# Optimization experiments

Measured on AMD Instinct MI355X. Metric: run time of the kernel, lower is better.

## Reference

```python
import jax, jax.numpy as jnp
import numpy as np
from functools import partial

B, T_OUT, T_IN, L, D_IN, D_ATT = 8, 256, 512, 128, 128, 128


def setup_inputs() -> dict:
    key = jax.random.key(0)
    ks = jax.random.split(key, 8)
    s = 0.05  # small init scale for numerical stability
    return {
        "inputs": jax.random.normal(ks[0], (B, T_OUT, D_IN), jnp.float32),
        "attended_inputs": jax.random.normal(ks[1], (B, T_IN, D_ATT), jnp.float32),
        "lstm_kernel": jax.random.normal(ks[2], (D_IN, 4 * L), jnp.float32) * s,
        "lstm_rec_kernel": jax.random.normal(ks[3], (L, 4 * L), jnp.float32) * s,
        "lstm_bias": jnp.zeros((4 * L,), jnp.float32),
        "W1": jax.random.normal(ks[4], (D_ATT, L), jnp.float32) * s,
        "b1": jnp.zeros((L,), jnp.float32),
        "W2": jax.random.normal(ks[5], (L, L), jnp.float32) * s,
        "b2": jnp.zeros((L,), jnp.float32),
        "W3": jax.random.normal(ks[6], (L, 1), jnp.float32) * s,
        "b3": jnp.zeros((1,), jnp.float32),
    }


def _lstm(x, Wk, Wr, b):
    # x: (B, T, D_in). Keras gate order: i, f, c(g), o. Zero initial state.
    Bq = x.shape[0]
    h0 = jnp.zeros((Bq, L), x.dtype)
    c0 = jnp.zeros((Bq, L), x.dtype)
    xz = jnp.einsum('btd,dk->btk', x, Wk) + b  # precompute input projection

    def step(carry, zt):
        h, c = carry
        z = zt + h @ Wr
        i, f, g, o = jnp.split(z, 4, axis=-1)
        c_new = jax.nn.sigmoid(f) * c + jax.nn.sigmoid(i) * jnp.tanh(g)
        h_new = jax.nn.sigmoid(o) * jnp.tanh(c_new)
        return (h_new, c_new), h_new

    (h_T, c_T), hs = jax.lax.scan(step, (h0, c0), jnp.swapaxes(xz, 0, 1))
    return jnp.swapaxes(hs, 0, 1), h_T, c_T  # (B, T, L), (B, L), (B, L)


def reference(inputs, attended_inputs, lstm_kernel, lstm_rec_kernel, lstm_bias,
              W1, b1, W2, b2, W3, b3):
    # setup_attended: keys = dense1(attended_inputs)
    keys = attended_inputs @ W1 + b1  # (B, T_in, L)
    x, h, c = _lstm(inputs, lstm_kernel, lstm_rec_kernel, lstm_bias)  # (B, T_out, L)
    q = x @ W2 + b2  # (B, T_out, L)
    # Bahdanau additive score: tanh(keys[:,None] + q[:,:,None]) . W3 -> (B, T_out, T_in)
    t = jnp.tanh(keys[:, None, :, :] + q[:, :, None, :])  # (B, T_out, T_in, L)
    scores = jnp.einsum('bqkl,l->bqk', t, W3[:, 0]) + b3[0]
    attn = jax.nn.softmax(scores, axis=-1)
    weighted = jnp.einsum('bqk,bkd->bqd', attn, attended_inputs)  # (B, T_out, D_att)
    out = jnp.concatenate([x, weighted], axis=2)  # (B, T_out, L + D_att)
    return out, h, c
```

## Files before the change

### kernel.cpp

```cpp
#include <hip/hip_runtime.h>
#include <hip/hip_bf16.h>

#define XF_OFF   0
#define PROG_OFF 524288
#define XZ_OFF   1048576
#define KEYS_OFF 2097152
#define OUT_H    524288
#define OUT_C    525312

#define LDS_BARRIER() __asm__ __volatile__("s_waitcnt lgkmcnt(0)\n\ts_barrier" ::: "memory")

#if __has_builtin(__builtin_amdgcn_exp2f)
#define EXP2F __builtin_amdgcn_exp2f
#else
#define EXP2F exp2f
#endif

typedef _Float16 f16x8 __attribute__((ext_vector_type(8)));
typedef float fx4 __attribute__((ext_vector_type(4)));

__device__ __forceinline__ float fast_rcp(float x) { return __builtin_amdgcn_rcpf(x); }
__device__ __forceinline__ float fast_sig(float v) { return fast_rcp(1.f + __expf(-v)); }
__device__ __forceinline__ float fast_tanh(float v) { return 2.f * fast_rcp(1.f + __expf(-2.f * v)) - 1.f; }

#define CSCALE (-2.8853900817779268f)

__global__ __launch_bounds__(256)
void prologue_k(const float* __restrict__ inp, const float* __restrict__ Wk,
                const float* __restrict__ bias, const float* __restrict__ att,
                const float* __restrict__ W1, const float* __restrict__ b1,
                float* __restrict__ ws) {
  __shared__ float ar[8][128];
  __shared__ float ar2[16][128];
  const int tid = threadIdx.x;

  if (blockIdx.x < 256) {
    _Float16* xz16 = (_Float16*)(ws + XZ_OFF);
    const int row0 = blockIdx.x * 8;
    for (int i = tid; i < 8 * 128; i += 256) ar[i >> 7][i & 127] = inp[row0 * 128 + i];
    __syncthreads();
    float acc[8][2];
    const float bb0 = bias[tid], bb1 = bias[tid + 256];
#pragma unroll
    for (int r = 0; r < 8; ++r) { acc[r][0] = bb0; acc[r][1] = bb1; }
    for (int d = 0; d < 128; d += 4) {
      float w0a = Wk[(d + 0) * 512 + tid], w0b = Wk[(d + 0) * 512 + tid + 256];
      float w1a = Wk[(d + 1) * 512 + tid], w1b = Wk[(d + 1) * 512 + tid + 256];
      float w2a = Wk[(d + 2) * 512 + tid], w2b = Wk[(d + 2) * 512 + tid + 256];
      float w3a = Wk[(d + 3) * 512 + tid], w3b = Wk[(d + 3) * 512 + tid + 256];
#pragma unroll
      for (int r = 0; r < 8; ++r) {
        float4 a4 = *(const float4*)&ar[r][d];
        acc[r][0] += a4.x * w0a + a4.y * w1a + a4.z * w2a + a4.w * w3a;
        acc[r][1] += a4.x * w0b + a4.y * w1b + a4.z * w2b + a4.w * w3b;
      }
    }
    const int u = tid & 127, g0 = tid >> 7;
#pragma unroll
    for (int r = 0; r < 8; ++r) {
      const int row = row0 + r, b = row >> 8, t = row & 255;
      const int base = ((t * 8 + b) * 128 + u) * 4;
      xz16[base + g0]     = (_Float16)acc[r][0];
      xz16[base + g0 + 2] = (_Float16)acc[r][1];
    }
    return;
  }

  if (blockIdx.x == 256 && tid < 2) ((int*)(ws + PROG_OFF))[tid] = 0;
  const int kb = blockIdx.x - 256;
  const int row0 = kb * 16;
  const int bq = row0 >> 9, k0 = row0 & 511;
  for (int i = tid; i < 16 * 128; i += 256) ar2[i >> 7][i & 127] = att[row0 * 128 + i];
  __syncthreads();
  const int l = tid & 127, r0 = tid >> 7;
  float acc[8];
  const float bl = b1[l];
#pragma unroll
  for (int i = 0; i < 8; ++i) acc[i] = bl;
  for (int d = 0; d < 128; d += 4) {
    float w0 = W1[(d + 0) * 128 + l], w1 = W1[(d + 1) * 128 + l];
    float w2 = W1[(d + 2) * 128 + l], w3 = W1[(d + 3) * 128 + l];
#pragma unroll
    for (int i = 0; i < 8; ++i) {
      float4 a4 = *(const float4*)&ar2[r0 * 8 + i][d];
      acc[i] += a4.x * w0 + a4.y * w1 + a4.z * w2 + a4.w * w3;
    }
  }
  float* kT = ws + KEYS_OFF + (bq * 128 + l) * 512 + k0 + r0 * 8;
  float4 lo = {acc[0], acc[1], acc[2], acc[3]};
  float4 hi = {acc[4], acc[5], acc[6], acc[7]};
  *(float4*)kT = lo;
  *(float4*)(kT + 4) = hi;
}

struct ScanS { _Float16 hb[2][576]; };
struct AttnS {
  float xr[4][128];
  float qp[4][128];
  float sc[4][512];
  float kc[8][516];
  float w3s[128];
};

__global__ __launch_bounds__(512)
void fused_scan_attn(const float* __restrict__ Wrf, const float* __restrict__ att,
                     const float* __restrict__ W2c, const float* __restrict__ b2c,
                     const float* __restrict__ W3c, const float* __restrict__ b3c,
                     float* __restrict__ ws, float* __restrict__ out) {
  __shared__ __align__(16) char smem[29312];
  const int tid = threadIdx.x;
  int* prog = (int*)(ws + PROG_OFF);
  float* xf = ws + XF_OFF;

  if (blockIdx.x == 256 || blockIdx.x == 257) return;

  if (blockIdx.x >= 2) {
    AttnS* A = (AttnS*)smem;
    const int wkr = (blockIdx.x < 256) ? (int)blockIdx.x - 2 : (int)blockIdx.x - 4;
    int cA = wkr, cB = 511 - wkr;
    if ((cA & 63) > (cB & 63)) { int tmp = cA; cA = cB; cB = tmp; }
    if (tid < 128) A->w3s[tid] = 2.f * W3c[tid];
    float sw3 = 0.f;
    for (int ll = 0; ll < 128; ll += 4) {
      float4 w4 = *(const float4*)&W3c[ll];
      sw3 += w4.x + w4.y + w4.z + w4.w;
    }
    const int l = tid & 127, r0 = tid >> 7;
    for (int ci = 0; ci < 2; ++ci) {
      const int c = ci ? cB : cA;
      const int b = c >> 6, q0 = (c & 63) * 4;
      if (tid == 0) {
        while (__hip_atomic_load(&prog[b >> 2], __ATOMIC_RELAXED, __HIP_MEMORY_SCOPE_AGENT) < q0 + 4)
          __builtin_amdgcn_s_sleep(16);
      }
      __syncthreads();
      const int row = b * 256 + q0 + r0;
      const float xv = __hip_atomic_load(&xf[row * 128 + l], __ATOMIC_RELAXED, __HIP_MEMORY_SCOPE_AGENT);
      A->xr[r0][l] = xv;
      out[row * 256 + l] = xv;
      __syncthreads();
      float qa = b2c[l];
      for (int d = 0; d < 128; d += 4) {
        float4 x4 = *(const float4*)&A->xr[r0][d];
        qa += x4.x * W2c[(d + 0) * 128 + l] + x4.y * W2c[(d + 1) * 128 + l]
            + x4.z * W2c[(d + 2) * 128 + l] + x4.w * W2c[(d + 3) * 128 + l];
      }
      A->qp[r0][l] = CSCALE * qa;
      const float base = b3c[0] - sw3;
      float acc0 = base, acc1 = base, acc2 = base, acc3 = base;
      const float* keysT = ws + KEYS_OFF + b * (128 * 512);
      for (int cc = 0; cc < 128; cc += 8) {
        __syncthreads();
        for (int i = tid; i < 8 * 512; i += 512)
          A->kc[i >> 9][i & 511] = CSCALE * keysT[(cc + (i >> 9)) * 512 + (i & 511)];
        __syncthreads();
        for (int lp = 0; lp < 8; ++lp) {
          const float qv = A->qp[r0][cc + lp];
          const float wv = A->w3s[cc + lp];
          acc0 += fast_rcp(1.f + EXP2F(A->kc[lp][l]       + qv)) * wv;
          acc1 += fast_rcp(1.f + EXP2F(A->kc[lp][l + 128] + qv)) * wv;
          acc2 += fast_rcp(1.f + EXP2F(A->kc[lp][l + 256] + qv)) * wv;
          acc3 += fast_rcp(1.f + EXP2F(A->kc[lp][l + 384] + qv)) * wv;
        }
      }
      A->sc[r0][l]       = acc0;
      A->sc[r0][l + 128] = acc1;
      A->sc[r0][l + 256] = acc2;
      A->sc[r0][l + 384] = acc3;
      __syncthreads();
      {
        const int wave = tid >> 6, lane = tid & 63;
        if (wave < 4) {
          float v[8];
#pragma unroll
          for (int i = 0; i < 8; ++i) v[i] = A->sc[wave][lane + i * 64];
          float m = v[0];
#pragma unroll
          for (int i = 1; i < 8; ++i) m = fmaxf(m, v[i]);
#pragma unroll
          for (int off = 32; off > 0; off >>= 1) m = fmaxf(m, __shfl_xor(m, off));
          float e[8], s = 0.f;
#pragma unroll
          for (int i = 0; i < 8; ++i) { e[i] = __expf(v[i] - m); s += e[i]; }
#pragma unroll
          for (int off = 32; off > 0; off >>= 1) s += __shfl_xor(s, off);
          const float inv = fast_rcp(s);
#pragma unroll
          for (int i = 0; i < 8; ++i) A->sc[wave][lane + i * 64] = e[i] * inv;
        }
      }
      __syncthreads();
      const float* attb = att + b * (512 * 128);
      float wa = 0.f;
      for (int k = 0; k < 512; k += 4) {
        float4 p4 = *(const float4*)&A->sc[r0][k];
        wa += p4.x * attb[(k + 0) * 128 + l] + p4.y * attb[(k + 1) * 128 + l]
            + p4.z * attb[(k + 2) * 128 + l] + p4.w * attb[(k + 3) * 128 + l];
      }
      out[row * 256 + 128 + l] = wa;
    }
    return;
  }

  __builtin_amdgcn_s_setprio(1);
  ScanS* S = (ScanS*)smem;
  const _Float16* xz16 = (const _Float16*)(ws + XZ_OFF);
  const int b_base = blockIdx.x * 4;
  const int w = tid >> 6, lane = tid & 63;
  const int q = lane >> 4, p = lane & 15;
  const int b = p & 3, isel = p >> 2;
  const int u = 16 * w + 4 * isel + q;
  const int bg = b_base + b;

  f16x8 afr[4][4];
#pragma unroll
  for (int i = 0; i < 4; ++i) {
    const int col = (p & 3) * 128 + 16 * w + 4 * i + (p >> 2);
#pragma unroll
    for (int kt = 0; kt < 4; ++kt)
#pragma unroll
      for (int j = 0; j < 8; ++j)
        afr[i][kt][j] = (_Float16)Wrf[(kt * 32 + q * 8 + j) * 512 + col];
  }
  {
    _Float16* hp = &S->hb[0][0];
    for (int i = tid; i < 2 * 576; i += 512) hp[i] = (_Float16)0.f;
  }
  const fx4 zeroC = {0.f, 0.f, 0.f, 0.f};
  float cst = 0.f, hval = 0.f;
  const _Float16* xp = xz16 + (bg * 128 + u) * 4;
  uint2 pf0 = *(const uint2*)(xp);
  uint2 pf1 = *(const uint2*)(xp + 4096);
  uint2 pf2 = *(const uint2*)(xp + 8192);
  __syncthreads();

  const int brow = b * 144;
  for (int t = 0; t < 256; ++t) {
    const _Float16* hrow = &S->hb[t & 1][brow];
    f16x8 bfr[4];
#pragma unroll
    for (int kt = 0; kt < 4; ++kt)
      bfr[kt] = *(const f16x8*)&hrow[kt * 32 + q * 8];
    fx4 acc[4];
#pragma unroll
    for (int i = 0; i < 4; ++i)
      acc[i] = __builtin_amdgcn_mfma_f32_16x16x32_f16(afr[i][0], bfr[0], zeroC, 0, 0, 0);
#pragma unroll
    for (int kt = 1; kt < 4; ++kt)
#pragma unroll
      for (int i = 0; i < 4; ++i)
        acc[i] = __builtin_amdgcn_mfma_f32_16x16x32_f16(afr[i][kt], bfr[kt], acc[i], 0, 0, 0);

    float z[4];
#pragma unroll
    for (int r = 0; r < 4; ++r) {
      float s01 = (isel & 1) ? acc[1][r] : acc[0][r];
      float s23 = (isel & 1) ? acc[3][r] : acc[2][r];
      z[r] = (isel & 2) ? s23 : s01;
    }

    uint2 cur = pf0;
    pf0 = pf1; pf1 = pf2;

    const _Float16* cf = (const _Float16*)&cur;
    const float zi = z[0] + (float)cf[0];
    const float zf = z[1] + (float)cf[1];
    const float zg = z[2] + (float)cf[2];
    const float zo = z[3] + (float)cf[3];
    cst = fast_sig(zf) * cst + fast_sig(zi) * fast_tanh(zg);
    hval = fast_sig(zo) * fast_tanh(cst);
    S->hb[(t + 1) & 1][brow + u] = (_Float16)hval;
    __hip_atomic_store(&xf[(bg * 256 + t) * 128 + u], hval,
                       __ATOMIC_RELAXED, __HIP_MEMORY_SCOPE_AGENT);

    if ((t & 31) == 31) {
      __syncthreads();
      if (tid == 0)
        __hip_atomic_store(&prog[blockIdx.x], t + 1,
                           __ATOMIC_RELAXED, __HIP_MEMORY_SCOPE_AGENT);
    } else {
      LDS_BARRIER();
    }
    const int t3 = (t + 3 < 256) ? t + 3 : 255;
    pf2 = *(const uint2*)(xp + t3 * 4096);
  }
  out[OUT_H + bg * 128 + u] = hval;
  out[OUT_C + bg * 128 + u] = cst;
}

extern "C" void kernel_launch(void* const* d_in, const int* in_sizes, int n_in,
                              void* d_out, int out_size, void* d_ws, size_t ws_size,
                              hipStream_t stream) {
  const float* inputs   = (const float*)d_in[0];
  const float* attended = (const float*)d_in[1];
  const float* Wk       = (const float*)d_in[2];
  const float* Wr       = (const float*)d_in[3];
  const float* bias     = (const float*)d_in[4];
  const float* W1       = (const float*)d_in[5];
  const float* b1       = (const float*)d_in[6];
  const float* W2       = (const float*)d_in[7];
  const float* b2       = (const float*)d_in[8];
  const float* W3       = (const float*)d_in[9];
  const float* b3       = (const float*)d_in[10];
  float* out = (float*)d_out;
  float* ws = (float*)d_ws;

  hipLaunchKernelGGL(prologue_k, dim3(512), dim3(256), 0, stream,
                     inputs, Wk, bias, attended, W1, b1, ws);
  hipLaunchKernelGGL(fused_scan_attn, dim3(260), dim3(512), 0, stream,
                     Wr, attended, W2, b2, W3, b3, ws, out);
}
```

Measured before the change: 329.6 us.

## Move keys projection into attention blocks and read keys directly from global

The keys projection (attended @ W1) is moved out of the prologue kernel and into the attention worker blocks of the fused kernel. Each worker computes a 16-row slice, pre-scales it, stores it transposed through shared memory, and bumps a per-batch completion counter that consumers spin on before scoring. The score loop no longer stages key chunks in LDS with barriers and instead reads keys straight from global/L2, which also shrinks LDS use. The aim is to overlap the keys work with the LSTM scan and cut prologue time and barrier count, at the cost of extra spin-wait synchronisation and uncached global reads in the inner loop.

```diff
diff --git a/kernel.cpp b/kernel.cpp
--- a/kernel.cpp
+++ b/kernel.cpp
@@ -26,110 +26,117 @@
 #define CSCALE (-2.8853900817779268f)
 
 __global__ __launch_bounds__(256)
-void prologue_k(const float* __restrict__ inp, const float* __restrict__ Wk,
-                const float* __restrict__ bias, const float* __restrict__ att,
-                const float* __restrict__ W1, const float* __restrict__ b1,
-                float* __restrict__ ws) {
+void xz_k(const float* __restrict__ inp, const float* __restrict__ Wk,
+          const float* __restrict__ bias, float* __restrict__ ws) {
   __shared__ float ar[8][128];
-  __shared__ float ar2[16][128];
   const int tid = threadIdx.x;
-
-  if (blockIdx.x < 256) {
-    _Float16* xz16 = (_Float16*)(ws + XZ_OFF);
-    const int row0 = blockIdx.x * 8;
-    for (int i = tid; i < 8 * 128; i += 256) ar[i >> 7][i & 127] = inp[row0 * 128 + i];
-    __syncthreads();
-    float acc[8][2];
-    const float bb0 = bias[tid], bb1 = bias[tid + 256];
-#pragma unroll
-    for (int r = 0; r < 8; ++r) { acc[r][0] = bb0; acc[r][1] = bb1; }
-    for (int d = 0; d < 128; d += 4) {
-      float w0a = Wk[(d + 0) * 512 + tid], w0b = Wk[(d + 0) * 512 + tid + 256];
-      float w1a = Wk[(d + 1) * 512 + tid], w1b = Wk[(d + 1) * 512 + tid + 256];
-      float w2a = Wk[(d + 2) * 512 + tid], w2b = Wk[(d + 2) * 512 + tid + 256];
-      float w3a = Wk[(d + 3) * 512 + tid], w3b = Wk[(d + 3) * 512 + tid + 256];
-#pragma unroll
-      for (int r = 0; r < 8; ++r) {
-        float4 a4 = *(const float4*)&ar[r][d];
-        acc[r][0] += a4.x * w0a + a4.y * w1a + a4.z * w2a + a4.w * w3a;
-        acc[r][1] += a4.x * w0b + a4.y * w1b + a4.z * w2b + a4.w * w3b;
-      }
-    }
-    const int u = tid & 127, g0 = tid >> 7;
+  if (blockIdx.x == 0 && tid < 10) ((int*)(ws + PROG_OFF))[tid] = 0;
+  _Float16* xz16 = (_Float16*)(ws + XZ_OFF);
+  const int row0 = blockIdx.x * 8;
+  for (int i = tid; i < 8 * 128; i += 256) ar[i >> 7][i & 127] = inp[row0 * 128 + i];
+  __syncthreads();
+  float acc[8][2];
+  const float bb0 = bias[tid], bb1 = bias[tid + 256];
+#pragma unroll
+  for (int r = 0; r < 8; ++r) { acc[r][0] = bb0; acc[r][1] = bb1; }
+  for (int d = 0; d < 128; d += 4) {
+    float w0a = Wk[(d + 0) * 512 + tid], w0b = Wk[(d + 0) * 512 + tid + 256];
+    float w1a = Wk[(d + 1) * 512 + tid], w1b = Wk[(d + 1) * 512 + tid + 256];
+    float w2a = Wk[(d + 2) * 512 + tid], w2b = Wk[(d + 2) * 512 + tid + 256];
+    float w3a = Wk[(d + 3) * 512 + tid], w3b = Wk[(d + 3) * 512 + tid + 256];
 #pragma unroll
     for (int r = 0; r < 8; ++r) {
-      const int row = row0 + r, b = row >> 8, t = row & 255;
-      const int base = ((t * 8 + b) * 128 + u) * 4;
-      xz16[base + g0]     = (_Float16)acc[r][0];
-      xz16[base + g0 + 2] = (_Float16)acc[r][1];
-    }
-    return;
-  }
-
-  if (blockIdx.x == 256 && tid < 2) ((int*)(ws + PROG_OFF))[tid] = 0;
-  const int kb = blockIdx.x - 256;
-  const int row0 = kb * 16;
-  const int bq = row0 >> 9, k0 = row0 & 511;
-  for (int i = tid; i < 16 * 128; i += 256) ar2[i >> 7][i & 127] = att[row0 * 128 + i];
-  __syncthreads();
-  const int l = tid & 127, r0 = tid >> 7;
-  float acc[8];
-  const float bl = b1[l];
-#pragma unroll
-  for (int i = 0; i < 8; ++i) acc[i] = bl;
-  for (int d = 0; d < 128; d += 4) {
-    float w0 = W1[(d + 0) * 128 + l], w1 = W1[(d + 1) * 128 + l];
-    float w2 = W1[(d + 2) * 128 + l], w3 = W1[(d + 3) * 128 + l];
-#pragma unroll
-    for (int i = 0; i < 8; ++i) {
-      float4 a4 = *(const float4*)&ar2[r0 * 8 + i][d];
-      acc[i] += a4.x * w0 + a4.y * w1 + a4.z * w2 + a4.w * w3;
-    }
-  }
-  float* kT = ws + KEYS_OFF + (bq * 128 + l) * 512 + k0 + r0 * 8;
-  float4 lo = {acc[0], acc[1], acc[2], acc[3]};
-  float4 hi = {acc[4], acc[5], acc[6], acc[7]};
-  *(float4*)kT = lo;
-  *(float4*)(kT + 4) = hi;
+      float4 a4 = *(const float4*)&ar[r][d];
+      acc[r][0] += a4.x * w0a + a4.y * w1a + a4.z * w2a + a4.w * w3a;
+      acc[r][1] += a4.x * w0b + a4.y * w1b + a4.z * w2b + a4.w * w3b;
+    }
+  }
+  const int u = tid & 127, g0 = tid >> 7;
+#pragma unroll
+  for (int r = 0; r < 8; ++r) {
+    const int row = row0 + r, b = row >> 8, t = row & 255;
+    const int base = ((t * 8 + b) * 128 + u) * 4;
+    xz16[base + g0]     = (_Float16)acc[r][0];
+    xz16[base + g0 + 2] = (_Float16)acc[r][1];
+  }
 }
 
-struct ScanS { _Float16 hb[2][576]; };
 struct AttnS {
   float xr[4][128];
   float qp[4][128];
   float sc[4][512];
-  float kc[8][516];
   float w3s[128];
 };
+struct KeyS { float st[16][132]; };
+struct KeyT { float tt[128][20]; };
+struct ScanS { _Float16 hb[2][576]; };
 
 __global__ __launch_bounds__(512)
 void fused_scan_attn(const float* __restrict__ Wrf, const float* __restrict__ att,
+                     const float* __restrict__ W1, const float* __restrict__ b1,
                      const float* __restrict__ W2c, const float* __restrict__ b2c,
                      const float* __restrict__ W3c, const float* __restrict__ b3c,
                      float* __restrict__ ws, float* __restrict__ out) {
-  __shared__ __align__(16) char smem[29312];
+  __shared__ __align__(16) char smem[12800];
   const int tid = threadIdx.x;
   int* prog = (int*)(ws + PROG_OFF);
+  int* kd = prog + 2;
   float* xf = ws + XF_OFF;
 
   if (blockIdx.x == 256 || blockIdx.x == 257) return;
 
   if (blockIdx.x >= 2) {
+    const int wkr = (blockIdx.x < 256) ? (int)blockIdx.x - 2 : (int)blockIdx.x - 4;
+    {
+      KeyS* K = (KeyS*)smem;
+      const int row0 = wkr * 16, bq = wkr >> 5, k0 = row0 & 511;
+      for (int i = tid; i < 16 * 128; i += 512) K->st[i >> 7][i & 127] = att[row0 * 128 + i];
+      __syncthreads();
+      const int l = tid & 127, r0 = tid >> 7;
+      float acc[4];
+      const float bl = b1[l];
+#pragma unroll
+      for (int i = 0; i < 4; ++i) acc[i] = bl;
+      for (int d = 0; d < 128; d += 4) {
+        float w0 = W1[(d + 0) * 128 + l], w1 = W1[(d + 1) * 128 + l];
+        float w2 = W1[(d + 2) * 128 + l], w3 = W1[(d + 3) * 128 + l];
+#pragma unroll
+        for (int i = 0; i < 4; ++i) {
+          float4 a4 = *(const float4*)&K->st[r0 * 4 + i][d];
+          acc[i] += a4.x * w0 + a4.y * w1 + a4.z * w2 + a4.w * w3;
+        }
+      }
+      __syncthreads();
+      KeyT* T = (KeyT*)smem;
+#pragma unroll
+      for (int i = 0; i < 4; ++i) T->tt[l][r0 * 4 + i] = CSCALE * acc[i];
+      __syncthreads();
+      const int l2 = tid >> 2, kq = tid & 3;
+      float* dst = ws + KEYS_OFF + (bq * 128 + l2) * 512 + k0 + kq * 4;
+      const float* srcv = &T->tt[l2][kq * 4];
+#pragma unroll
+      for (int j = 0; j < 4; ++j)
+        __hip_atomic_store(dst + j, srcv[j], __ATOMIC_RELAXED, __HIP_MEMORY_SCOPE_AGENT);
+      __syncthreads();
+      if (tid == 0)
+        __hip_atomic_fetch_add(&kd[bq], 1, __ATOMIC_RELAXED, __HIP_MEMORY_SCOPE_AGENT);
+    }
     AttnS* A = (AttnS*)smem;
-    const int wkr = (blockIdx.x < 256) ? (int)blockIdx.x - 2 : (int)blockIdx.x - 4;
-    int cA = wkr, cB = 511 - wkr;
-    if ((cA & 63) > (cB & 63)) { int tmp = cA; cA = cB; cB = tmp; }
     if (tid < 128) A->w3s[tid] = 2.f * W3c[tid];
     float sw3 = 0.f;
     for (int ll = 0; ll < 128; ll += 4) {
       float4 w4 = *(const float4*)&W3c[ll];
       sw3 += w4.x + w4.y + w4.z + w4.w;
     }
+    int cA = wkr, cB = 511 - wkr;
+    if ((cA & 63) > (cB & 63)) { int tmp = cA; cA = cB; cB = tmp; }
     const int l = tid & 127, r0 = tid >> 7;
     for (int ci = 0; ci < 2; ++ci) {
       const int c = ci ? cB : cA;
       const int b = c >> 6, q0 = (c & 63) * 4;
       if (tid == 0) {
+        while (__hip_atomic_load(&kd[b], __ATOMIC_RELAXED, __HIP_MEMORY_SCOPE_AGENT) < 32)
+          __builtin_amdgcn_s_sleep(8);
         while (__hip_atomic_load(&prog[b >> 2], __ATOMIC_RELAXED, __HIP_MEMORY_SCOPE_AGENT) < q0 + 4)
           __builtin_amdgcn_s_sleep(16);
       }
@@ -146,22 +153,19 @@
             + x4.z * W2c[(d + 2) * 128 + l] + x4.w * W2c[(d + 3) * 128 + l];
       }
       A->qp[r0][l] = CSCALE * qa;
+      __syncthreads();
       const float base = b3c[0] - sw3;
       float acc0 = base, acc1 = base, acc2 = base, acc3 = base;
-      const float* keysT = ws + KEYS_OFF + b * (128 * 512);
-      for (int cc = 0; cc < 128; cc += 8) {
-        __syncthreads();
-        for (int i = tid; i < 8 * 512; i += 512)
-          A->kc[i >> 9][i & 511] = CSCALE * keysT[(cc + (i >> 9)) * 512 + (i & 511)];
-        __syncthreads();
-        for (int lp = 0; lp < 8; ++lp) {
-          const float qv = A->qp[r0][cc + lp];
-          const float wv = A->w3s[cc + lp];
-          acc0 += fast_rcp(1.f + EXP2F(A->kc[lp][l]       + qv)) * wv;
-          acc1 += fast_rcp(1.f + EXP2F(A->kc[lp][l + 128] + qv)) * wv;
-          acc2 += fast_rcp(1.f + EXP2F(A->kc[lp][l + 256] + qv)) * wv;
-          acc3 += fast_rcp(1.f + EXP2F(A->kc[lp][l + 384] + qv)) * wv;
-        }
+      const float* kr = ws + KEYS_OFF + b * (128 * 512) + l;
+#pragma unroll 4
+      for (int lc = 0; lc < 128; ++lc) {
+        const float qv = A->qp[r0][lc];
+        const float wv = A->w3s[lc];
+        acc0 += fast_rcp(1.f + EXP2F(kr[0]   + qv)) * wv;
+        acc1 += fast_rcp(1.f + EXP2F(kr[128] + qv)) * wv;
+        acc2 += fast_rcp(1.f + EXP2F(kr[256] + qv)) * wv;
+        acc3 += fast_rcp(1.f + EXP2F(kr[384] + qv)) * wv;
+        kr += 512;
       }
       A->sc[r0][l]       = acc0;
       A->sc[r0][l + 128] = acc1;
@@ -305,8 +309,7 @@
   float* out = (float*)d_out;
   float* ws = (float*)d_ws;
 
-  hipLaunchKernelGGL(prologue_k, dim3(512), dim3(256), 0, stream,
-                     inputs, Wk, bias, attended, W1, b1, ws);
+  hipLaunchKernelGGL(xz_k, dim3(256), dim3(256), 0, stream, inputs, Wk, bias, ws);
   hipLaunchKernelGGL(fused_scan_attn, dim3(260), dim3(512), 0, stream,
-                     Wr, attended, W2, b2, W3, b3, ws, out);
+                     Wr, attended, W1, b1, W2, b2, W3, b3, ws, out);
 }
```

Measured after the change: 453.5 us. 1.38x slower.
